# Performance work log

Measured on AMD Instinct MI355X. Metric: run time of the kernel, lower is better.

The kernel has to match this reference:

```python
import jax, jax.numpy as jnp
import numpy as np

N = 8192
HID = 256
LAMBDA = 1.0
MU = 1.0
DIM = 2
GC = 0.0027
L = 0.02
Y0, Y1 = 0.0, 1.0
STRESS_PRE_SCALE = 1.0
PF_PRE_SCALE = 1.0


def loading(t):
    # linear displacement loading
    return t[0]


def mlp(Ws, bs, inp):
    h = inp
    for W, b in zip(Ws[:-1], bs[:-1]):
        h = jnp.tanh(h @ W + b)
    return h @ Ws[-1] + bs[-1]


def net_u(Ws, bs, x, t):
    sol = mlp(Ws, bs, jnp.concatenate([x, t]))  # (3,)
    phi = jax.nn.sigmoid(sol[:1])               # (1,)
    ld = loading(t)
    ux = (x[1] - Y0) * (x[1] - Y1) * sol[1:2] * ld / 3.0
    uy = (x[1] - Y0) * (x[1] - Y1) * sol[2:3] * ld + (x[1] - Y0) / (Y1 - Y0) * ld
    return phi, jnp.concatenate([ux, uy])       # (1,), (2,)


def epsilon_fn(Ws, bs, x, t):
    J = jax.jacrev(lambda xx: net_u(Ws, bs, xx, t)[1])(x)  # (2,2)
    return (J + J.T) / 2.0


def psi_pos(eps):
    tr = jnp.trace(eps)
    k = LAMBDA + MU * 2.0 / DIM
    dev = eps - tr * jnp.eye(DIM, dtype=eps.dtype) / DIM
    return k * jax.nn.relu(tr) ** 2 / 2 + MU * jnp.trace(dev @ dev)


def psi_neg(eps):
    k = LAMBDA + MU * 2.0 / DIM
    return k * jax.nn.relu(-jnp.trace(eps)) ** 2 / 2


def sigma_fn(Ws, bs, x, t):
    phi, _ = net_u(Ws, bs, x, t)
    g_phi = (1 - phi[0]) ** 2 + 1e-6
    eps = epsilon_fn(Ws, bs, x, t)
    return g_phi * jax.grad(psi_pos)(eps) + jax.grad(psi_neg)(eps)


def net_stress(Ws, bs, x, t):
    def damaged(xx):
        phi, _ = net_u(Ws, bs, xx, t)
        return (1 - phi) ** 2 * sigma_fn(Ws, bs, xx, t)  # (2,2)
    D = jax.jacrev(damaged)(x)          # (2,2,2)
    return jnp.einsum('ijj->i', D) / STRESS_PRE_SCALE


def net_pf_raw(Ws, bs, x, t):
    phi, _ = net_u(Ws, bs, x, t)
    phi0 = phi[0]
    eps = epsilon_fn(Ws, bs, x, t)
    H = jax.hessian(lambda xx: net_u(Ws, bs, xx, t)[0])(x)[0]  # (2,2)
    lap_phi = jnp.trace(H)
    pf = GC * (phi0 / L - L * lap_phi) - 2 * (1 - phi0) * psi_pos(eps)
    return pf / PF_PRE_SCALE


def net_speed(Ws, bs, x, t):
    return jax.jacrev(lambda tt: net_u(Ws, bs, x, tt)[0])(t)[0, 0]


def net_pf(Ws, bs, x, t):
    pf = net_pf_raw(Ws, bs, x, t)
    dphi_dt = net_speed(Ws, bs, x, t)
    phi0 = net_u(Ws, bs, x, t)[0][0]
    mask_pos = (jnp.abs(dphi_dt) <= 1e-3) & (jnp.abs(phi0 - 1) > 1e-3)
    mask_neg = jnp.abs(phi0 - 1) <= 1e-3
    return jnp.where(mask_pos, jax.nn.relu(-pf), jnp.where(mask_neg, jax.nn.relu(pf), pf))


def net_energy(Ws, bs, x, t):
    phi0 = net_u(Ws, bs, x, t)[0][0]
    eps = epsilon_fn(Ws, bs, x, t)
    nphi = jax.jacrev(lambda xx: net_u(Ws, bs, xx, t)[0])(x)[0]  # (2,)
    return ((1 - phi0) * 2 * psi_pos(eps) + psi_neg(eps)
            + GC * (phi0 ** 2 / (2 * L) + L / 2 * jnp.sum(nphi ** 2)))


def _forward(W0, W1, W2, W3, W4, b0, b1, b2, b3, b4, x, t):
    Ws = [W0, W1, W2, W3, W4]
    bs = [b0, b1, b2, b3, b4]
    res_s = jax.vmap(net_stress, in_axes=(None, None, 0, 0))(Ws, bs, x, t)   # (N,2)
    res_pf = jax.vmap(net_pf, in_axes=(None, None, 0, 0))(Ws, bs, x, t)     # (N,)
    res_e = jax.vmap(net_energy, in_axes=(None, None, 0, 0))(Ws, bs, x, t)  # (N,)
    dphi = jax.vmap(net_speed, in_axes=(None, None, 0, 0))(Ws, bs, x, t)    # (N,)
    # component re-weighting for the vector stress residual (as in loss_pde)
    mse_res = jnp.mean(res_s ** 2, axis=0)  # (2,)
    w = jax.lax.stop_gradient(jnp.mean(mse_res) / (mse_res + 1e-6))
    r = jnp.sqrt(jnp.sum(res_s ** 2 * w[None, :], axis=-1))
    loss_stress = jnp.mean(r ** 2)
    loss_pf = jnp.mean(res_pf ** 2)
    loss_energy = jnp.log(jnp.sum(res_e))
    loss_irr = jnp.mean(jax.nn.relu(-dphi))
    return jnp.stack([loss_stress, loss_pf, loss_energy, loss_irr])


def setup_inputs() -> dict:
    key = jax.random.key(0)
    dims = [3, HID, HID, HID, HID, 3]
    ks = jax.random.split(key, 12)
    inp = {}
    for i in range(5):
        fan_in, fan_out = dims[i], dims[i + 1]
        inp[f'W{i}'] = (jax.random.normal(ks[i], (fan_in, fan_out), jnp.float32)
                        * np.sqrt(2.0 / (fan_in + fan_out)).astype(np.float32))
        inp[f'b{i}'] = jnp.zeros((fan_out,), jnp.float32)
    inp['x'] = jax.random.uniform(ks[10], (N, 2), jnp.float32, 0.0, 1.0)
    inp['t'] = jax.random.uniform(ks[11], (N, 1), jnp.float32, 0.05, 1.0)
    return inp


def reference(W0, W1, W2, W3, W4, b0, b1, b2, b3, b4, x, t):
    return _forward(W0, W1, W2, W3, W4, b0, b1, b2, b3, b4, x, t)
```

## Files before the change

### kernel.cpp

```cpp
#include <hip/hip_runtime.h>
#include <math.h>

#define N_PTS 8192
#define HIDDEN 256
#define PPB 8
#define THREADS 256
#define NBLK (N_PTS / PPB)
#define NBINS 64
#define MROWS 56
#define LDA 264
#define BP_OFF 4096

typedef float f32x4 __attribute__((ext_vector_type(4)));
typedef short s8v  __attribute__((ext_vector_type(8)));

__device__ __forceinline__ unsigned short bf16_rne(float x) {
    unsigned int u = __float_as_uint(x);
    return (unsigned short)((u + 0x7FFFu + ((u >> 16) & 1u)) >> 16);
}
__device__ __forceinline__ float bf16f(unsigned short h) {
    return __uint_as_float(((unsigned int)h) << 16);
}

__global__ void pinn_pack(const float* __restrict__ W1, const float* __restrict__ W2,
                          const float* __restrict__ W3, unsigned short* __restrict__ Bp)
{
    const int id = blockIdx.x * 256 + threadIdx.x;
    const int lane = id & 63;
    const int nt   = (id >> 6) & 15;
    const int kc   = (id >> 10) & 7;
    const int l    = id >> 13;
    const float* W = (l == 0) ? W1 : ((l == 1) ? W2 : W3);
    const int n  = nt * 16 + (lane & 15);
    const int k0 = kc * 32 + (lane >> 4) * 8;
    unsigned short hi[8], lo[8];
    #pragma unroll
    for (int i = 0; i < 8; ++i) {
        const float x = W[(size_t)(k0 + i) * HIDDEN + n];
        const unsigned short h = bf16_rne(x);
        hi[i] = h;
        lo[i] = bf16_rne(x - bf16f(h));
    }
    const size_t bh = ((((size_t)(l * 2 + 0) * 8 + kc) * 16 + nt) * 64 + lane) * 8;
    const size_t bl = ((((size_t)(l * 2 + 1) * 8 + kc) * 16 + nt) * 64 + lane) * 8;
    *(s8v*)&Bp[bh] = *(const s8v*)hi;
    *(s8v*)&Bp[bl] = *(const s8v*)lo;
}

__global__ __launch_bounds__(THREADS, 2)
void pinn_main(const float* __restrict__ W0, const float* __restrict__ b0,
               const float* __restrict__ b1, const float* __restrict__ b2,
               const float* __restrict__ b3,
               const float* __restrict__ W4, const float* __restrict__ b4,
               const float* __restrict__ xin, const float* __restrict__ tin,
               const unsigned short* __restrict__ Bp,
               float* __restrict__ bins)
{
    __shared__ __align__(16) unsigned char LB[MROWS * LDA * 4];
    short* __restrict__ AhS = (short*)LB;
    short* __restrict__ AlS = (short*)(LB + MROWS * LDA * 2);
    float* __restrict__ Zf  = (float*)LB;

    const int tid  = threadIdx.x;
    const int lane = tid & 63;
    const int w    = tid >> 6;
    const int c    = lane & 15;
    const int g    = lane >> 4;
    const int t    = tid;
    const int pt0  = blockIdx.x * PPB;

    {
        const float w0 = W0[t], w1 = W0[HIDDEN + t], w2 = W0[2 * HIDDEN + t];
        const float bb = b0[t];
        for (int p = 0; p < PPB; ++p) {
            const float x0 = xin[(pt0 + p) * 2 + 0];
            const float x1 = xin[(pt0 + p) * 2 + 1];
            const float tt = tin[pt0 + p];
            const float z  = fmaf(x0, w0, fmaf(x1, w1, fmaf(tt, w2, bb)));
            const float a  = tanhf(z);
            const float st = 1.f - a * a;
            const float m2 = -2.f * a * st;
            float v[7];
            v[0] = a;
            v[1] = st * w0; v[2] = st * w1; v[3] = st * w2;
            v[4] = m2 * w0 * w0; v[5] = m2 * w0 * w1; v[6] = m2 * w1 * w1;
            #pragma unroll
            for (int s = 0; s < 7; ++s) {
                const int r = 8 * s + p;
                const unsigned short h = bf16_rne(v[s]);
                AhS[r * LDA + t] = (short)h;
                AlS[r * LDA + t] = (short)bf16_rne(v[s] - bf16f(h));
            }
        }
    }
    __syncthreads();

    int aoff[4];
    #pragma unroll
    for (int mt = 0; mt < 4; ++mt) {
        int arow = mt * 16 + c;
        if (arow > MROWS - 1) arow = MROWS - 1;
        aoff[mt] = arow * LDA + g * 8;
    }

    for (int l = 0; l < 3; ++l) {
        f32x4 acc[4][4];
        #pragma unroll
        for (int mt = 0; mt < 4; ++mt)
            #pragma unroll
            for (int nn = 0; nn < 4; ++nn) acc[mt][nn] = (f32x4)0.f;

        const size_t lbase = (size_t)l * 2 * 8 * 16 * 64 * 8;
        for (int kc = 0; kc < 8; ++kc) {
            s8v ah[4], al[4];
            #pragma unroll
            for (int mt = 0; mt < 4; ++mt) {
                ah[mt] = *(const s8v*)&AhS[aoff[mt] + kc * 32];
                al[mt] = *(const s8v*)&AlS[aoff[mt] + kc * 32];
            }
            s8v bh[4], bl[4];
            #pragma unroll
            for (int nn = 0; nn < 4; ++nn) {
                const int nt = w * 4 + nn;
                const size_t oh = lbase + (((size_t)kc * 16 + nt) * 64 + lane) * 8;
                const size_t ol = oh + (size_t)8 * 16 * 64 * 8;
                bh[nn] = *(const s8v*)&Bp[oh];
                bl[nn] = *(const s8v*)&Bp[ol];
            }
            #pragma unroll
            for (int mt = 0; mt < 4; ++mt)
                #pragma unroll
                for (int nn = 0; nn < 4; ++nn) {
                    acc[mt][nn] = __builtin_amdgcn_mfma_f32_16x16x32_bf16(ah[mt], bh[nn], acc[mt][nn], 0, 0, 0);
                    acc[mt][nn] = __builtin_amdgcn_mfma_f32_16x16x32_bf16(ah[mt], bl[nn], acc[mt][nn], 0, 0, 0);
                    acc[mt][nn] = __builtin_amdgcn_mfma_f32_16x16x32_bf16(al[mt], bh[nn], acc[mt][nn], 0, 0, 0);
                }
        }
        __syncthreads();

        #pragma unroll
        for (int mt = 0; mt < 4; ++mt)
            #pragma unroll
            for (int nn = 0; nn < 4; ++nn)
                #pragma unroll
                for (int r = 0; r < 4; ++r) {
                    const int row = mt * 16 + g * 4 + r;
                    if (row < MROWS)
                        Zf[row * LDA + w * 64 + nn * 16 + c] = acc[mt][nn][r];
                }
        __syncthreads();

        float zr[MROWS];
        #pragma unroll
        for (int r = 0; r < MROWS; ++r) zr[r] = Zf[r * LDA + t];
        __syncthreads();

        const float bias = ((l == 0) ? b1 : (l == 1) ? b2 : b3)[t];
        for (int p = 0; p < PPB; ++p) {
            const float zv = zr[p] + bias;
            const float a  = tanhf(zv);
            const float st = 1.f - a * a;
            const float m2 = -2.f * a * st;
            const float z1 = zr[8 + p],  z2 = zr[16 + p], z3 = zr[24 + p];
            const float z4 = zr[32 + p], z5 = zr[40 + p], z6 = zr[48 + p];
            float v[7];
            v[0] = a;
            v[1] = st * z1; v[2] = st * z2; v[3] = st * z3;
            v[4] = fmaf(m2 * z1, z1, st * z4);
            v[5] = fmaf(m2 * z1, z2, st * z5);
            v[6] = fmaf(m2 * z2, z2, st * z6);
            if (l < 2) {
                #pragma unroll
                for (int s = 0; s < 7; ++s) {
                    const int r = 8 * s + p;
                    const unsigned short h = bf16_rne(v[s]);
                    AhS[r * LDA + t] = (short)h;
                    AlS[r * LDA + t] = (short)bf16_rne(v[s] - bf16f(h));
                }
            } else {
                #pragma unroll
                for (int s = 0; s < 7; ++s)
                    Zf[(8 * s + p) * LDA + t] = v[s];
            }
        }
        __syncthreads();
    }

    const int h  = (lane >> 5);
    const int la = lane & 31;
    const int p  = w * 2 + h;

    float part[7][3];
    #pragma unroll
    for (int s = 0; s < 7; ++s)
        #pragma unroll
        for (int m = 0; m < 3; ++m) part[s][m] = 0.f;

    #pragma unroll
    for (int i = 0; i < 8; ++i) {
        const int k = la + 32 * i;
        const float w40 = W4[k * 3 + 0], w41 = W4[k * 3 + 1], w42 = W4[k * 3 + 2];
        #pragma unroll
        for (int s = 0; s < 7; ++s) {
            const float hk = Zf[(8 * s + p) * LDA + k];
            part[s][0] = fmaf(hk, w40, part[s][0]);
            part[s][1] = fmaf(hk, w41, part[s][1]);
            part[s][2] = fmaf(hk, w42, part[s][2]);
        }
    }
    #pragma unroll
    for (int s = 0; s < 7; ++s)
        #pragma unroll
        for (int m = 0; m < 3; ++m) {
            float v = part[s][m];
            #pragma unroll
            for (int off = 16; off > 0; off >>= 1) v += __shfl_xor(v, off);
            part[s][m] = v;
        }

    const float x0 = xin[(pt0 + p) * 2 + 0];
    const float x1 = xin[(pt0 + p) * 2 + 1];
    const float tt = tin[pt0 + p];

    const float V0 = part[0][0] + b4[0];
    const float V1 = part[0][1] + b4[1];
    const float V2 = part[0][2] + b4[2];
    const float J00 = part[1][0], J01 = part[2][0], J0t = part[3][0];
    const float J10 = part[1][1], J11 = part[2][1];
    const float J20 = part[1][2], J21 = part[2][2];
    const float H000 = part[4][0], H011 = part[6][0];
    const float H100 = part[4][1], H101 = part[5][1], H111 = part[6][1];
    const float H200 = part[4][2], H201 = part[5][2], H211 = part[6][2];

    const float phi = 1.f / (1.f + expf(-V0));
    const float om  = 1.f - phi;
    const float sp  = phi * om;
    const float spp = sp * (1.f - 2.f * phi);
    const float phx0 = sp * J00, phx1 = sp * J01, dphidt = sp * J0t;
    const float lap = spp * (J00 * J00 + J01 * J01) + sp * (H000 + H011);

    const float ld = tt;
    const float q = x1 * (x1 - 1.f), qp = 2.f * x1 - 1.f;

    const float ux0 = q * J10 * ld * (1.f / 3.f);
    const float ux1 = (qp * V1 + q * J11) * ld * (1.f / 3.f);
    const float uy0 = q * J20 * ld;
    const float uy1 = (qp * V2 + q * J21) * ld + ld;

    const float e00 = ux0, e11 = uy1, e01 = 0.5f * (ux1 + uy0);
    const float tr = e00 + e11;

    const float ux_00 = q * H100 * ld * (1.f / 3.f);
    const float ux_01 = (qp * J10 + q * H101) * ld * (1.f / 3.f);
    const float ux_11 = (2.f * V1 + 2.f * qp * J11 + q * H111) * ld * (1.f / 3.f);
    const float uy_00 = q * H200 * ld;
    const float uy_01 = (qp * J20 + q * H201) * ld;
    const float uy_11 = (2.f * V2 + 2.f * qp * J21 + q * H211) * ld;

    const float de00_0 = ux_00, de00_1 = ux_01;
    const float de11_0 = uy_01, de11_1 = uy_11;
    const float de01_0 = 0.5f * (ux_01 + uy_00), de01_1 = 0.5f * (ux_11 + uy_01);
    const float dtr_0 = de00_0 + de11_0, dtr_1 = de00_1 + de11_1;

    const float kk = 2.f;
    const float rtr = fmaxf(tr, 0.f), rntr = fmaxf(-tr, 0.f);
    const float Hp = (tr > 0.f) ? 1.f : 0.f, Hn = (tr < 0.f) ? 1.f : 0.f;

    const float dv = 0.5f * (e00 - e11);
    const float sp00 = kk * rtr + 2.f * dv;
    const float sp11 = kk * rtr - 2.f * dv;
    const float sp01 = 2.f * e01;
    const float snd  = -kk * rntr;

    const float dsp00_0 = kk * Hp * dtr_0 + 2.f * (de00_0 - 0.5f * dtr_0);
    const float dsp01_0 = 2.f * de01_0;
    const float dsp01_1 = 2.f * de01_1;
    const float dsp11_1 = kk * Hp * dtr_1 + 2.f * (de11_1 - 0.5f * dtr_1);
    const float dsn_0 = kk * Hn * dtr_0, dsn_1 = kk * Hn * dtr_1;

    const float cc  = om * om, gg = cc + 1e-6f;
    const float dc0 = -2.f * om * phx0, dc1 = -2.f * om * phx1;
    const float gpc = gg + cc, cg = cc * gg;

    const float res0 = dc0 * gpc * sp00 + cg * dsp00_0 + dc0 * snd + cc * dsn_0
                     + dc1 * gpc * sp01 + cg * dsp01_1;
    const float res1 = dc0 * gpc * sp01 + cg * dsp01_0
                     + dc1 * gpc * sp11 + cg * dsp11_1 + dc1 * snd + cc * dsn_1;

    const float psip = rtr * rtr + 0.5f * (e00 - e11) * (e00 - e11) + 2.f * e01 * e01;
    const float psin = rntr * rntr;

    const float GCc = 0.0027f, LL = 0.02f;
    const float pf = GCc * (phi / LL - LL * lap) - 2.f * om * psip;
    const bool maskp = (fabsf(dphidt) <= 1e-3f) && (fabsf(phi - 1.f) > 1e-3f);
    const bool maskn = fabsf(phi - 1.f) <= 1e-3f;
    const float respf = maskp ? fmaxf(-pf, 0.f) : (maskn ? fmaxf(pf, 0.f) : pf);

    const float rese = om * 2.f * psip + psin
                     + GCc * (phi * phi / (2.f * LL)
                              + 0.5f * LL * (phx0 * phx0 + phx1 * phx1));
    const float irr = fmaxf(-dphidt, 0.f);

    if (la == 0) {
        float* bin = bins + (blockIdx.x & (NBINS - 1)) * 8;
        atomicAdd(bin + 0, res0 * res0);
        atomicAdd(bin + 1, res1 * res1);
        atomicAdd(bin + 2, respf * respf);
        atomicAdd(bin + 3, rese);
        atomicAdd(bin + 4, irr);
    }
}

__global__ void pinn_finalize(const float* __restrict__ bins, float* __restrict__ out)
{
    if (threadIdx.x == 0 && blockIdx.x == 0) {
        float S[5] = {0.f, 0.f, 0.f, 0.f, 0.f};
        for (int b = 0; b < NBINS; ++b)
            for (int k = 0; k < 5; ++k) S[k] += bins[b * 8 + k];
        const float inv_n = 1.f / (float)N_PTS;
        const float mse0 = S[0] * inv_n, mse1 = S[1] * inv_n;
        const float wm = 0.5f * (mse0 + mse1);
        out[0] = wm * mse0 / (mse0 + 1e-6f) + wm * mse1 / (mse1 + 1e-6f);
        out[1] = S[2] * inv_n;
        out[2] = logf(S[3]);
        out[3] = S[4] * inv_n;
    }
}

extern "C" void kernel_launch(void* const* d_in, const int* in_sizes, int n_in,
                              void* d_out, int out_size, void* d_ws, size_t ws_size,
                              hipStream_t stream)
{
    const float *W[5], *b[5];
    if (in_sizes[1] == HIDDEN) {
        for (int i = 0; i < 5; ++i) {
            W[i] = (const float*)d_in[2 * i];
            b[i] = (const float*)d_in[2 * i + 1];
        }
    } else {
        for (int i = 0; i < 5; ++i) {
            W[i] = (const float*)d_in[i];
            b[i] = (const float*)d_in[5 + i];
        }
    }
    const float* x = (const float*)d_in[10];
    const float* t = (const float*)d_in[11];
    float* bins = (float*)d_ws;
    unsigned short* Bp = (unsigned short*)((char*)d_ws + BP_OFF);

    hipMemsetAsync(bins, 0, NBINS * 8 * sizeof(float), stream);
    pinn_pack<<<96, 256, 0, stream>>>(W[1], W[2], W[3], Bp);
    pinn_main<<<NBLK, THREADS, 0, stream>>>(W[0], b[0], b[1], b[2], b[3],
                                            W[4], b[4], x, t, Bp, bins);
    pinn_finalize<<<1, 64, 0, stream>>>(bins, (float*)d_out);
}
```

Before: 165.9 us.

## Vectorize activation LDS traffic, fold memset into pack, parallelize finalize

Each thread now handles 4 hidden units for 2 points instead of one unit for 8 points, so activation and derivative rows are read and written to LDS with 4-wide vector accesses. The Z buffer gets a separate stride of 260 floats. The k-chunk MFMA loop is fully unrolled. The hipMemset is replaced by zeroing the bins inside the pack kernel, and finalize uses a wave shuffle reduction. Together these aim to cut LDS instruction count, launch overhead and serial reduction time, at the cost of higher register pressure and possible LDS bank conflicts from the new stride.

```diff
diff --git a/kernel.cpp b/kernel.cpp
--- a/kernel.cpp
+++ b/kernel.cpp
@@ -9,10 +9,12 @@
 #define NBINS 64
 #define MROWS 56
 #define LDA 264
+#define LDZ 260
 #define BP_OFF 4096
 
 typedef float f32x4 __attribute__((ext_vector_type(4)));
 typedef short s8v  __attribute__((ext_vector_type(8)));
+typedef short s4v  __attribute__((ext_vector_type(4)));
 
 __device__ __forceinline__ unsigned short bf16_rne(float x) {
     unsigned int u = __float_as_uint(x);
@@ -23,8 +25,13 @@
 }
 
 __global__ void pinn_pack(const float* __restrict__ W1, const float* __restrict__ W2,
-                          const float* __restrict__ W3, unsigned short* __restrict__ Bp)
+                          const float* __restrict__ W3, unsigned short* __restrict__ Bp,
+                          float* __restrict__ bins)
 {
+    if (blockIdx.x == 0) {
+        bins[threadIdx.x] = 0.f;
+        bins[threadIdx.x + 256] = 0.f;
+    }
     const int id = blockIdx.x * 256 + threadIdx.x;
     const int lane = id & 63;
     const int nt   = (id >> 6) & 15;
@@ -66,30 +73,46 @@
     const int w    = tid >> 6;
     const int c    = lane & 15;
     const int g    = lane >> 4;
-    const int t    = tid;
+    const int q    = tid & 63;
+    const int pp   = tid >> 6;
     const int pt0  = blockIdx.x * PPB;
 
     {
-        const float w0 = W0[t], w1 = W0[HIDDEN + t], w2 = W0[2 * HIDDEN + t];
-        const float bb = b0[t];
-        for (int p = 0; p < PPB; ++p) {
+        const f32x4 w0 = *(const f32x4*)(W0 + q * 4);
+        const f32x4 w1 = *(const f32x4*)(W0 + HIDDEN + q * 4);
+        const f32x4 w2 = *(const f32x4*)(W0 + 2 * HIDDEN + q * 4);
+        const f32x4 bb = *(const f32x4*)(b0 + q * 4);
+        #pragma unroll
+        for (int p2 = 0; p2 < 2; ++p2) {
+            const int p = pp + 4 * p2;
             const float x0 = xin[(pt0 + p) * 2 + 0];
             const float x1 = xin[(pt0 + p) * 2 + 1];
             const float tt = tin[pt0 + p];
-            const float z  = fmaf(x0, w0, fmaf(x1, w1, fmaf(tt, w2, bb)));
-            const float a  = tanhf(z);
-            const float st = 1.f - a * a;
-            const float m2 = -2.f * a * st;
-            float v[7];
-            v[0] = a;
-            v[1] = st * w0; v[2] = st * w1; v[3] = st * w2;
-            v[4] = m2 * w0 * w0; v[5] = m2 * w0 * w1; v[6] = m2 * w1 * w1;
+            s4v hi[7], lo[7];
+            #pragma unroll
+            for (int jj = 0; jj < 4; ++jj) {
+                const float z  = fmaf(x0, w0[jj], fmaf(x1, w1[jj], fmaf(tt, w2[jj], bb[jj])));
+                const float a  = tanhf(z);
+                const float st = 1.f - a * a;
+                const float m2 = -2.f * a * st;
+                float v[7];
+                v[0] = a;
+                v[1] = st * w0[jj]; v[2] = st * w1[jj]; v[3] = st * w2[jj];
+                v[4] = m2 * w0[jj] * w0[jj];
+                v[5] = m2 * w0[jj] * w1[jj];
+                v[6] = m2 * w1[jj] * w1[jj];
+                #pragma unroll
+                for (int s = 0; s < 7; ++s) {
+                    const unsigned short h = bf16_rne(v[s]);
+                    hi[s][jj] = (short)h;
+                    lo[s][jj] = (short)bf16_rne(v[s] - bf16f(h));
+                }
+            }
             #pragma unroll
             for (int s = 0; s < 7; ++s) {
                 const int r = 8 * s + p;
-                const unsigned short h = bf16_rne(v[s]);
-                AhS[r * LDA + t] = (short)h;
-                AlS[r * LDA + t] = (short)bf16_rne(v[s] - bf16f(h));
+                *(s4v*)&AhS[r * LDA + q * 4] = hi[s];
+                *(s4v*)&AlS[r * LDA + q * 4] = lo[s];
             }
         }
     }
@@ -111,6 +134,7 @@
             for (int nn = 0; nn < 4; ++nn) acc[mt][nn] = (f32x4)0.f;
 
         const size_t lbase = (size_t)l * 2 * 8 * 16 * 64 * 8;
+        #pragma unroll
         for (int kc = 0; kc < 8; ++kc) {
             s8v ah[4], al[4];
             #pragma unroll
@@ -146,41 +170,63 @@
                 for (int r = 0; r < 4; ++r) {
                     const int row = mt * 16 + g * 4 + r;
                     if (row < MROWS)
-                        Zf[row * LDA + w * 64 + nn * 16 + c] = acc[mt][nn][r];
+                        Zf[row * LDZ + w * 64 + nn * 16 + c] = acc[mt][nn][r];
                 }
         __syncthreads();
 
-        float zr[MROWS];
-        #pragma unroll
-        for (int r = 0; r < MROWS; ++r) zr[r] = Zf[r * LDA + t];
+        f32x4 z[2][7];
+        #pragma unroll
+        for (int p2 = 0; p2 < 2; ++p2) {
+            const int p = pp + 4 * p2;
+            #pragma unroll
+            for (int s = 0; s < 7; ++s)
+                z[p2][s] = *(const f32x4*)&Zf[(8 * s + p) * LDZ + q * 4];
+        }
         __syncthreads();
 
-        const float bias = ((l == 0) ? b1 : (l == 1) ? b2 : b3)[t];
-        for (int p = 0; p < PPB; ++p) {
-            const float zv = zr[p] + bias;
-            const float a  = tanhf(zv);
-            const float st = 1.f - a * a;
-            const float m2 = -2.f * a * st;
-            const float z1 = zr[8 + p],  z2 = zr[16 + p], z3 = zr[24 + p];
-            const float z4 = zr[32 + p], z5 = zr[40 + p], z6 = zr[48 + p];
-            float v[7];
-            v[0] = a;
-            v[1] = st * z1; v[2] = st * z2; v[3] = st * z3;
-            v[4] = fmaf(m2 * z1, z1, st * z4);
-            v[5] = fmaf(m2 * z1, z2, st * z5);
-            v[6] = fmaf(m2 * z2, z2, st * z6);
+        const float* bias = (l == 0) ? b1 : (l == 1) ? b2 : b3;
+        const f32x4 bb = *(const f32x4*)(bias + q * 4);
+        #pragma unroll
+        for (int p2 = 0; p2 < 2; ++p2) {
+            const int p = pp + 4 * p2;
+            s4v hi[7], lo[7];
+            f32x4 vf[7];
+            #pragma unroll
+            for (int jj = 0; jj < 4; ++jj) {
+                const float zv = z[p2][0][jj] + bb[jj];
+                const float a  = tanhf(zv);
+                const float st = 1.f - a * a;
+                const float m2 = -2.f * a * st;
+                const float z1 = z[p2][1][jj], z2 = z[p2][2][jj], z3 = z[p2][3][jj];
+                float v[7];
+                v[0] = a;
+                v[1] = st * z1; v[2] = st * z2; v[3] = st * z3;
+                v[4] = fmaf(m2 * z1, z1, st * z[p2][4][jj]);
+                v[5] = fmaf(m2 * z1, z2, st * z[p2][5][jj]);
+                v[6] = fmaf(m2 * z2, z2, st * z[p2][6][jj]);
+                if (l < 2) {
+                    #pragma unroll
+                    for (int s = 0; s < 7; ++s) {
+                        const unsigned short h = bf16_rne(v[s]);
+                        hi[s][jj] = (short)h;
+                        lo[s][jj] = (short)bf16_rne(v[s] - bf16f(h));
+                    }
+                } else {
+                    #pragma unroll
+                    for (int s = 0; s < 7; ++s) vf[s][jj] = v[s];
+                }
+            }
             if (l < 2) {
                 #pragma unroll
                 for (int s = 0; s < 7; ++s) {
                     const int r = 8 * s + p;
-                    const unsigned short h = bf16_rne(v[s]);
-                    AhS[r * LDA + t] = (short)h;
-                    AlS[r * LDA + t] = (short)bf16_rne(v[s] - bf16f(h));
+                    *(s4v*)&AhS[r * LDA + q * 4] = hi[s];
+                    *(s4v*)&AlS[r * LDA + q * 4] = lo[s];
                 }
             } else {
                 #pragma unroll
                 for (int s = 0; s < 7; ++s)
-                    Zf[(8 * s + p) * LDA + t] = v[s];
+                    *(f32x4*)&Zf[(8 * s + p) * LDZ + q * 4] = vf[s];
             }
         }
         __syncthreads();
@@ -202,7 +248,7 @@
         const float w40 = W4[k * 3 + 0], w41 = W4[k * 3 + 1], w42 = W4[k * 3 + 2];
         #pragma unroll
         for (int s = 0; s < 7; ++s) {
-            const float hk = Zf[(8 * s + p) * LDA + k];
+            const float hk = Zf[(8 * s + p) * LDZ + k];
             part[s][0] = fmaf(hk, w40, part[s][0]);
             part[s][1] = fmaf(hk, w41, part[s][1]);
             part[s][2] = fmaf(hk, w42, part[s][2]);
@@ -240,22 +286,22 @@
     const float lap = spp * (J00 * J00 + J01 * J01) + sp * (H000 + H011);
 
     const float ld = tt;
-    const float q = x1 * (x1 - 1.f), qp = 2.f * x1 - 1.f;
-
-    const float ux0 = q * J10 * ld * (1.f / 3.f);
-    const float ux1 = (qp * V1 + q * J11) * ld * (1.f / 3.f);
-    const float uy0 = q * J20 * ld;
-    const float uy1 = (qp * V2 + q * J21) * ld + ld;
+    const float qq = x1 * (x1 - 1.f), qp = 2.f * x1 - 1.f;
+
+    const float ux0 = qq * J10 * ld * (1.f / 3.f);
+    const float ux1 = (qp * V1 + qq * J11) * ld * (1.f / 3.f);
+    const float uy0 = qq * J20 * ld;
+    const float uy1 = (qp * V2 + qq * J21) * ld + ld;
 
     const float e00 = ux0, e11 = uy1, e01 = 0.5f * (ux1 + uy0);
     const float tr = e00 + e11;
 
-    const float ux_00 = q * H100 * ld * (1.f / 3.f);
-    const float ux_01 = (qp * J10 + q * H101) * ld * (1.f / 3.f);
-    const float ux_11 = (2.f * V1 + 2.f * qp * J11 + q * H111) * ld * (1.f / 3.f);
-    const float uy_00 = q * H200 * ld;
-    const float uy_01 = (qp * J20 + q * H201) * ld;
-    const float uy_11 = (2.f * V2 + 2.f * qp * J21 + q * H211) * ld;
+    const float ux_00 = qq * H100 * ld * (1.f / 3.f);
+    const float ux_01 = (qp * J10 + qq * H101) * ld * (1.f / 3.f);
+    const float ux_11 = (2.f * V1 + 2.f * qp * J11 + qq * H111) * ld * (1.f / 3.f);
+    const float uy_00 = qq * H200 * ld;
+    const float uy_01 = (qp * J20 + qq * H201) * ld;
+    const float uy_11 = (2.f * V2 + 2.f * qp * J21 + qq * H211) * ld;
 
     const float de00_0 = ux_00, de00_1 = ux_01;
     const float de11_0 = uy_01, de11_1 = uy_11;
@@ -313,17 +359,28 @@
 
 __global__ void pinn_finalize(const float* __restrict__ bins, float* __restrict__ out)
 {
-    if (threadIdx.x == 0 && blockIdx.x == 0) {
-        float S[5] = {0.f, 0.f, 0.f, 0.f, 0.f};
-        for (int b = 0; b < NBINS; ++b)
-            for (int k = 0; k < 5; ++k) S[k] += bins[b * 8 + k];
+    const int lane = threadIdx.x;
+    float s0 = bins[lane * 8 + 0];
+    float s1 = bins[lane * 8 + 1];
+    float s2 = bins[lane * 8 + 2];
+    float s3 = bins[lane * 8 + 3];
+    float s4 = bins[lane * 8 + 4];
+    #pragma unroll
+    for (int off = 32; off > 0; off >>= 1) {
+        s0 += __shfl_xor(s0, off);
+        s1 += __shfl_xor(s1, off);
+        s2 += __shfl_xor(s2, off);
+        s3 += __shfl_xor(s3, off);
+        s4 += __shfl_xor(s4, off);
+    }
+    if (lane == 0) {
         const float inv_n = 1.f / (float)N_PTS;
-        const float mse0 = S[0] * inv_n, mse1 = S[1] * inv_n;
+        const float mse0 = s0 * inv_n, mse1 = s1 * inv_n;
         const float wm = 0.5f * (mse0 + mse1);
         out[0] = wm * mse0 / (mse0 + 1e-6f) + wm * mse1 / (mse1 + 1e-6f);
-        out[1] = S[2] * inv_n;
-        out[2] = logf(S[3]);
-        out[3] = S[4] * inv_n;
+        out[1] = s2 * inv_n;
+        out[2] = logf(s3);
+        out[3] = s4 * inv_n;
     }
 }
 
@@ -348,8 +405,7 @@
     float* bins = (float*)d_ws;
     unsigned short* Bp = (unsigned short*)((char*)d_ws + BP_OFF);
 
-    hipMemsetAsync(bins, 0, NBINS * 8 * sizeof(float), stream);
-    pinn_pack<<<96, 256, 0, stream>>>(W[1], W[2], W[3], Bp);
+    pinn_pack<<<96, 256, 0, stream>>>(W[1], W[2], W[3], Bp, bins);
     pinn_main<<<NBLK, THREADS, 0, stream>>>(W[0], b[0], b[1], b[2], b[3],
                                             W[4], b[4], x, t, Bp, bins);
     pinn_finalize<<<1, 64, 0, stream>>>(bins, (float*)d_out);
```

Measured after the change: 161.6 us. 2.6% less time.
